# Performance work log

Hardware: AMD Instinct MI355X
Metric: run time of the kernel (lower is better)

The kernel has to match this reference:

```python
import jax, jax.numpy as jnp
import numpy as np

H, C = 8, 640            # n_heads, sentence_size (per-head out channels)
HC = H * C               # 5120 concatenated head width
NS, NW, NSEC = 8192, 65536, 1024   # sentences, words, sections
EW, ES, ESEC = 131072, 262144, 16384
WORD, SENT, SECT = 300, 640, 512
FFN_HID = 2048


def setup_inputs() -> dict:
    key = jax.random.key(0)
    ks = jax.random.split(key, 32)
    f = lambda k, sh: (jax.random.normal(k, sh, jnp.float32) * 0.02)
    ri = jax.random.randint
    inp = {}
    inp['Hs'] = jax.random.normal(ks[0], (NS, SENT), jnp.float32)
    inp['Hw'] = jax.random.normal(ks[1], (NW, WORD), jnp.float32)
    inp['HS'] = jax.random.normal(ks[2], (NSEC, SECT), jnp.float32)
    # edge_index convention: row 0 = source nodes, row 1 = target (sentence) nodes
    inp['w2s'] = jnp.stack([ri(ks[3], (EW,), 0, NW), ri(ks[4], (EW,), 0, NS)]).astype(jnp.int32)
    inp['s2s'] = jnp.stack([ri(ks[5], (ES,), 0, NS), ri(ks[6], (ES,), 0, NS)]).astype(jnp.int32)
    inp['S2s'] = jnp.stack([ri(ks[7], (ESEC,), 0, NSEC), ri(ks[8], (ESEC,), 0, NS)]).astype(jnp.int32)
    # gat_w: bipartite (word -> sentence)
    inp['Ww_src'] = f(ks[9], (WORD, HC)); inp['Ww_dst'] = f(ks[10], (SENT, HC))
    inp['aw_src'] = f(ks[11], (H, C)); inp['aw_dst'] = f(ks[12], (H, C)); inp['bw'] = f(ks[13], (HC,))
    # gat_s: sentence -> sentence (shared lin for src/dst)
    inp['Ws'] = f(ks[14], (SENT, HC))
    inp['as_src'] = f(ks[15], (H, C)); inp['as_dst'] = f(ks[16], (H, C)); inp['bs'] = f(ks[17], (HC,))
    # gat_S: bipartite (section -> sentence)
    inp['WS_src'] = f(ks[18], (SECT, HC)); inp['WS_dst'] = f(ks[19], (SENT, HC))
    inp['aS_src'] = f(ks[20], (H, C)); inp['aS_dst'] = f(ks[21], (H, C)); inp['bS'] = f(ks[22], (HC,))
    # fusion gates
    inp['F1_w'] = f(ks[23], (2 * HC, HC)); inp['F1_b'] = f(ks[24], (HC,))
    inp['F2_w'] = f(ks[25], (2 * HC, HC)); inp['F2_b'] = f(ks[26], (HC,))
    # FFN
    inp['l1_w'] = f(ks[27], (HC, FFN_HID)); inp['l1_b'] = f(ks[28], (FFN_HID,))
    inp['l2_w'] = f(ks[29], (FFN_HID, SENT)); inp['l2_b'] = f(ks[30], (SENT,))
    return inp


def _gat(xs, xd, Wsrc, Wdst, asrc, adst, b, edge_index):
    """PyG-style GATConv (concat heads), bipartite (xs -> xd)."""
    N = xd.shape[0]
    hs = (xs @ Wsrc).reshape(-1, H, C)          # [Nsrc,H,C]
    hd = (xd @ Wdst).reshape(-1, H, C)          # [Ndst,H,C]
    al_s = jnp.einsum('nhc,hc->nh', hs, asrc)   # [Nsrc,H]
    al_d = jnp.einsum('nhc,hc->nh', hd, adst)   # [Ndst,H]
    src, dst = edge_index[0], edge_index[1]
    e = jax.nn.leaky_relu(al_s[src] + al_d[dst], negative_slope=0.2)  # [E,H]
    m = jax.ops.segment_max(e, dst, num_segments=N)                   # segment-stable softmax
    ex = jnp.exp(e - m[dst])
    den = jax.ops.segment_sum(ex, dst, num_segments=N)
    alpha = ex / (den[dst] + 1e-16)
    out = jax.ops.segment_sum(hs[src] * alpha[:, :, None], dst, num_segments=N)
    return out.reshape(N, HC) + b


def _fusion(X, Y, W, b):
    Z = jax.nn.sigmoid(jnp.concatenate([X, Y], axis=-1) @ W + b)
    return Z * X + (1.0 - Z) * Y


def reference(Hs, Hw, HS, w2s, s2s, S2s,
              Ww_src, Ww_dst, aw_src, aw_dst, bw,
              Ws, as_src, as_dst, bs,
              WS_src, WS_dst, aS_src, aS_dst, bS,
              F1_w, F1_b, F2_w, F2_b,
              l1_w, l1_b, l2_w, l2_b):
    Uw = jax.nn.elu(_gat(Hw, Hs, Ww_src, Ww_dst, aw_src, aw_dst, bw, w2s))
    Us = jax.nn.elu(_gat(Hs, Hs, Ws, Ws, as_src, as_dst, bs, s2s))
    US = jax.nn.elu(_gat(HS, Hs, WS_src, WS_dst, aS_src, aS_dst, bS, S2s))
    U1 = _fusion(Uw, Us, F1_w, F1_b)
    U2 = _fusion(U1, US, F2_w, F2_b)
    return (U2 @ l1_w + l1_b) @ l2_w + l2_b + Hs
```

## Files before the change

kernel.cpp:

```cpp
#include <hip/hip_runtime.h>
#include <cstdint>
#include <cstddef>

typedef __attribute__((ext_vector_type(8))) __bf16 bf16x8;
typedef __attribute__((ext_vector_type(4))) float f32x4;

static constexpr int kNS   = 8192;
static constexpr int kNW   = 65536;
static constexpr int kNSEC = 1024;
static constexpr int kEW   = 131072;
static constexpr int kES   = 262144;
static constexpr int kESEC = 16384;

__device__ __forceinline__ float eluf(float x)  { return x > 0.f ? x : (__expf(x) - 1.f); }
__device__ __forceinline__ float sigmf(float x) { return 1.f / (1.f + __expf(-x)); }

__device__ __forceinline__ void gload16(const __bf16* g, __bf16* l) {
  __builtin_amdgcn_global_load_lds((const __attribute__((address_space(1))) unsigned int*)g,
                                   (__attribute__((address_space(3))) unsigned int*)l,
                                   16, 0, 0);
}

__global__ __launch_bounds__(256) void conv_transpose(const float* __restrict__ W, int K, int N,
                                                      __bf16* __restrict__ Wt, int KP) {
  __shared__ float t[64][33];
  const int nb = blockIdx.x * 32, kb = blockIdx.y * 64;
  const int tx = threadIdx.x & 31, ty = threadIdx.x >> 5;
#pragma unroll
  for (int i = ty; i < 64; i += 8) {
    const int k = kb + i;
    t[i][tx] = (k < K) ? W[(long)k * N + nb + tx] : 0.f;
  }
  __syncthreads();
  union BU { __bf16 b; unsigned short u; };
#pragma unroll
  for (int i = ty; i < 32; i += 8) {
    BU b0, b1;
    b0.b = (__bf16)t[tx * 2][i];
    b1.b = (__bf16)t[tx * 2 + 1][i];
    const unsigned int pk = ((unsigned int)b1.u << 16) | b0.u;
    *(unsigned int*)(Wt + (long)(nb + i) * KP + kb + tx * 2) = pk;
  }
}

__global__ __launch_bounds__(256) void conv_bf(const float* __restrict__ in, __bf16* __restrict__ outb, long n) {
  long i = (long)blockIdx.x * blockDim.x + threadIdx.x;
  if (i < n) outb[i] = (__bf16)in[i];
}

struct HVJ { const float* W; const float* a; float* o; int Kd; int KP; };
struct HVJobs { HVJ j[6]; };

__global__ __launch_bounds__(256) void head_vecs6(HVJobs jb) {
  const HVJ J = jb.j[blockIdx.z];
  const int h = blockIdx.x;
  const int lane = threadIdx.x & 63;
  const int k = blockIdx.y * 4 + (threadIdx.x >> 6);
  if (k >= J.KP) return;
  float s = 0.f;
  if (k < J.Kd) {
    const float* wr = J.W + (long)k * 5120 + h * 640;
    const float* ar = J.a + h * 640;
    for (int c = lane; c < 640; c += 64) s += wr[c] * ar[c];
  }
  for (int o2 = 32; o2; o2 >>= 1) s += __shfl_down(s, o2);
  if (lane == 0) J.o[h * J.KP + k] = (k < J.Kd) ? s : 0.f;
}

__global__ __launch_bounds__(256) void comb_bias(const float* __restrict__ l1_b, const float* __restrict__ l2_w,
                                                 const float* __restrict__ l2_b, float* __restrict__ bc) {
  const int n = blockIdx.x * 256 + threadIdx.x;
  if (n >= 640) return;
  float s = l2_b[n];
  for (int k = 0; k < 2048; ++k) s += l1_b[k] * l2_w[(long)k * 640 + n];
  bc[n] = s;
}

__global__ __launch_bounds__(256) void att_logits(const float* __restrict__ X, int ldx, int Kd,
                                                  const float* __restrict__ vec, int KP,
                                                  float* __restrict__ outl, int N) {
  const int lane = threadIdx.x & 63;
  const int node = blockIdx.x * 4 + (threadIdx.x >> 6);
  if (node >= N) return;
  const float* xr = X + (long)node * ldx;
  float p[8];
#pragma unroll
  for (int h = 0; h < 8; ++h) p[h] = 0.f;
  for (int k = lane; k < Kd; k += 64) {
    const float xv = xr[k];
#pragma unroll
    for (int h = 0; h < 8; ++h) p[h] += xv * vec[h * KP + k];
  }
#pragma unroll
  for (int h = 0; h < 8; ++h) {
    float v = p[h];
    for (int o2 = 32; o2; o2 >>= 1) v += __shfl_down(v, o2);
    if (lane == 0) outl[(long)node * 8 + h] = v;
  }
}

__global__ __launch_bounds__(256) void att_logits4(const float* __restrict__ X,
                                                   const float* __restrict__ v0, const float* __restrict__ v1,
                                                   const float* __restrict__ v2, const float* __restrict__ v3,
                                                   float* __restrict__ o0, float* __restrict__ o1,
                                                   float* __restrict__ o2, float* __restrict__ o3, int N) {
  const int lane = threadIdx.x & 63;
  const int node = blockIdx.x * 4 + (threadIdx.x >> 6);
  if (node >= N) return;
  const float* xr = X + (long)node * 640;
  float p[4][8];
#pragma unroll
  for (int s = 0; s < 4; ++s)
#pragma unroll
    for (int h = 0; h < 8; ++h) p[s][h] = 0.f;
  for (int k = lane; k < 640; k += 64) {
    const float xv = xr[k];
#pragma unroll
    for (int h = 0; h < 8; ++h) {
      p[0][h] += xv * v0[h * 640 + k];
      p[1][h] += xv * v1[h * 640 + k];
      p[2][h] += xv * v2[h * 640 + k];
      p[3][h] += xv * v3[h * 640 + k];
    }
  }
  float* outs[4] = {o0, o1, o2, o3};
#pragma unroll
  for (int s = 0; s < 4; ++s)
#pragma unroll
    for (int h = 0; h < 8; ++h) {
      float v = p[s][h];
      for (int o2v = 32; o2v; o2v >>= 1) v += __shfl_down(v, o2v);
      if (lane == 0) outs[s][(long)node * 8 + h] = v;
    }
}

__global__ __launch_bounds__(256) void edge_count3(const int* __restrict__ d0, int E0, int* __restrict__ c0,
                                                   const int* __restrict__ d1, int E1, int* __restrict__ c1,
                                                   const int* __restrict__ d2, int E2, int* __restrict__ c2) {
  const int gid = blockIdx.x * blockDim.x + threadIdx.x;
  if (gid < E0) atomicAdd(&c0[d0[gid]], 1);
  else if (gid < E0 + E1) atomicAdd(&c1[d1[gid - E0]], 1);
  else if (gid < E0 + E1 + E2) atomicAdd(&c2[d2[gid - E0 - E1]], 1);
}

__global__ __launch_bounds__(1024) void scan_off3(const int* __restrict__ c0, int* __restrict__ o0,
                                                  const int* __restrict__ c1, int* __restrict__ o1,
                                                  const int* __restrict__ c2, int* __restrict__ o2) {
  const int* cnt = blockIdx.x == 0 ? c0 : (blockIdx.x == 1 ? c1 : c2);
  int* offo = blockIdx.x == 0 ? o0 : (blockIdx.x == 1 ? o1 : o2);
  __shared__ int part[1024];
  const int tid = threadIdx.x;
  const int base = tid * 8;
  int loc[8];
  int s = 0;
#pragma unroll
  for (int i = 0; i < 8; ++i) { loc[i] = s; s += cnt[base + i]; }
  part[tid] = s;
  __syncthreads();
  for (int d2 = 1; d2 < 1024; d2 <<= 1) {
    int v = (tid >= d2) ? part[tid - d2] : 0;
    __syncthreads();
    part[tid] += v;
    __syncthreads();
  }
  const int pre = (tid > 0) ? part[tid - 1] : 0;
#pragma unroll
  for (int i = 0; i < 8; ++i) offo[base + i] = pre + loc[i];
  if (tid == 1023) offo[8192] = part[1023];
}

__global__ __launch_bounds__(256) void edge_fill3(
    const int* __restrict__ s0, const int* __restrict__ d0, int E0, const int* __restrict__ of0, int* __restrict__ cu0, int* __restrict__ sr0,
    const int* __restrict__ s1, const int* __restrict__ d1, int E1, const int* __restrict__ of1, int* __restrict__ cu1, int* __restrict__ sr1,
    const int* __restrict__ s2, const int* __restrict__ d2, int E2, const int* __restrict__ of2, int* __restrict__ cu2, int* __restrict__ sr2) {
  const int gid = blockIdx.x * blockDim.x + threadIdx.x;
  if (gid < E0) {
    const int d = d0[gid];
    sr0[of0[d] + atomicAdd(&cu0[d], 1)] = s0[gid];
  } else if (gid < E0 + E1) {
    const int g = gid - E0, d = d1[g];
    sr1[of1[d] + atomicAdd(&cu1[d], 1)] = s1[g];
  } else if (gid < E0 + E1 + E2) {
    const int g = gid - E0 - E1, d = d2[g];
    sr2[of2[d] + atomicAdd(&cu2[d], 1)] = s2[g];
  }
}

template <int FPAD, int F, bool XPH, bool BIASELU>
__global__ __launch_bounds__(256) void gat_agg(const int* __restrict__ seg_off, const int* __restrict__ ssrc,
                                               const float* __restrict__ als, const float* __restrict__ ald,
                                               const float* __restrict__ X, int ldx,
                                               __bf16* __restrict__ outp, int ldo,
                                               const float* __restrict__ bias) {
  constexpr int C4 = F / 4;
  constexpr int ITEMS = 8 * C4;
  constexpr int L = (ITEMS + 255) / 256;
  const int d = blockIdx.x;
  const int tid = threadIdx.x;
  const int o0 = seg_off[d], o1 = seg_off[d + 1];
  const int deg = o1 - o0;
  __shared__ float exl[64][8];
  __shared__ int ssl[64];
  __shared__ float aldd[8];
  __shared__ float den_s[8];
  if (tid < 8) { aldd[tid] = ald[(long)d * 8 + tid]; den_s[tid] = 0.f; }
  f32x4 acc[L];
  int hh[L], xo[L], oo[L];
  bool vld[L];
#pragma unroll
  for (int l = 0; l < L; ++l) {
    const int idx = tid + l * 256;
    vld[l] = (idx < ITEMS);
    const int h = vld[l] ? (idx / C4) : 0;
    const int c = vld[l] ? (idx - h * C4) : 0;
    hh[l] = h;
    xo[l] = (XPH ? h * F : 0) + c * 4;
    oo[l] = h * FPAD + c * 4;
#pragma unroll
    for (int r = 0; r < 4; ++r) acc[l][r] = 0.f;
  }
  __syncthreads();
  for (int base = 0; base < deg; base += 64) {
    const int nc = min(64, deg - base);
    if (tid < nc) ssl[tid] = ssrc[o0 + base + tid];
    __syncthreads();
    for (int t = tid; t < nc * 8; t += 256) {
      const int e = t >> 3, h = t & 7;
      float v = als[(long)ssl[e] * 8 + h] + aldd[h];
      v = v > 0.f ? v : 0.2f * v;
      exl[e][h] = __expf(v);
    }
    __syncthreads();
    if (tid < 8) {
      float s = 0.f;
      for (int e = 0; e < nc; ++e) s += exl[e][tid];
      den_s[tid] += s;
    }
    for (int e = 0; e < nc; ++e) {
      const float* xr = X + (long)ssl[e] * ldx;
      const float* ex8 = exl[e];
#pragma unroll
      for (int l = 0; l < L; ++l)
        if (vld[l]) {
          const f32x4 v = *(const f32x4*)(xr + xo[l]);
          acc[l] += ex8[hh[l]] * v;
        }
    }
    __syncthreads();
  }
#pragma unroll
  for (int l = 0; l < L; ++l) {
    if (!vld[l]) continue;
    const float dinv = 1.f / (den_s[hh[l]] + 1e-16f);
#pragma unroll
    for (int j = 0; j < 4; ++j) {
      float r = acc[l][j] * dinv;
      if constexpr (BIASELU) { r += bias[oo[l] + j]; r = eluf(r); }
      outp[(long)d * ldo + oo[l] + j] = (__bf16)r;
    }
  }
}

template <int FPAD, int F, bool XPH, bool BIASELU>
__global__ __launch_bounds__(256) void gat_agg_bf(const int* __restrict__ seg_off, const int* __restrict__ ssrc,
                                                  const float* __restrict__ als, const float* __restrict__ ald,
                                                  const __bf16* __restrict__ X, int ldx,
                                                  __bf16* __restrict__ outp, int ldo,
                                                  const float* __restrict__ bias) {
  constexpr int C8 = F / 8;
  constexpr int ITEMS = 8 * C8;
  constexpr int L = (ITEMS + 255) / 256;
  const int d = blockIdx.x;
  const int tid = threadIdx.x;
  const int o0 = seg_off[d], o1 = seg_off[d + 1];
  const int deg = o1 - o0;
  __shared__ float exl[64][8];
  __shared__ int ssl[64];
  __shared__ float aldd[8];
  __shared__ float den_s[8];
  if (tid < 8) { aldd[tid] = ald[(long)d * 8 + tid]; den_s[tid] = 0.f; }
  float acc[L][8];
  int hh[L], xo[L], oo[L];
  bool vld[L];
#pragma unroll
  for (int l = 0; l < L; ++l) {
    const int idx = tid + l * 256;
    vld[l] = (idx < ITEMS);
    const int h = vld[l] ? (idx / C8) : 0;
    const int c = vld[l] ? (idx - h * C8) : 0;
    hh[l] = h;
    xo[l] = (XPH ? h * F : 0) + c * 8;
    oo[l] = h * FPAD + c * 8;
#pragma unroll
    for (int r = 0; r < 8; ++r) acc[l][r] = 0.f;
  }
  __syncthreads();
  for (int base = 0; base < deg; base += 64) {
    const int nc = min(64, deg - base);
    if (tid < nc) ssl[tid] = ssrc[o0 + base + tid];
    __syncthreads();
    for (int t = tid; t < nc * 8; t += 256) {
      const int e = t >> 3, h = t & 7;
      float v = als[(long)ssl[e] * 8 + h] + aldd[h];
      v = v > 0.f ? v : 0.2f * v;
      exl[e][h] = __expf(v);
    }
    __syncthreads();
    if (tid < 8) {
      float s = 0.f;
      for (int e = 0; e < nc; ++e) s += exl[e][tid];
      den_s[tid] += s;
    }
    for (int e = 0; e < nc; ++e) {
      const __bf16* xr = X + (long)ssl[e] * ldx;
      const float* ex8 = exl[e];
#pragma unroll
      for (int l = 0; l < L; ++l)
        if (vld[l]) {
          const bf16x8 v = *(const bf16x8*)(xr + xo[l]);
          const float w = ex8[hh[l]];
#pragma unroll
          for (int r = 0; r < 8; ++r) acc[l][r] += w * (float)v[r];
        }
    }
    __syncthreads();
  }
#pragma unroll
  for (int l = 0; l < L; ++l) {
    if (!vld[l]) continue;
    const float dinv = 1.f / (den_s[hh[l]] + 1e-16f);
#pragma unroll
    for (int j = 0; j < 8; ++j) {
      float r = acc[l][j] * dinv;
      if constexpr (BIASELU) { r += bias[oo[l] + j]; r = eluf(r); }
      outp[(long)d * ldo + oo[l] + j] = (__bf16)r;
    }
  }
}

template <int EPI>
__global__ __launch_bounds__(256) void gemm_bt(
    const __bf16* __restrict__ A, int lda, const __bf16* __restrict__ A2, int ksplit,
    const __bf16* __restrict__ Bt, int ldb, int K,
    void* __restrict__ Cout, int ldc,
    const float* __restrict__ bias,
    const __bf16* __restrict__ Xg, const __bf16* __restrict__ Yg, int ldxy,
    const float* __restrict__ Res, int ldres,
    long a_zs, long bt_zs, long c_zs, int b_zs) {
  __shared__ __bf16 sA[2][128 * 32];
  __shared__ __bf16 sB[2][128 * 32];
  const int tid = threadIdx.x;
  const int z = blockIdx.z;
  const int m0 = blockIdx.y * 128, n0 = blockIdx.x * 128;
  const __bf16* Ab = A + (long)z * a_zs;
  const __bf16* A2b = A2 ? A2 + (long)z * a_zs : nullptr;
  const __bf16* Btb = Bt + (long)z * bt_zs;
  const int lane = tid & 63;
  const int wv = tid >> 6, wr = wv >> 1, wc = wv & 1;
  const int fr = lane & 15, fq = lane >> 4;

  const int r0 = tid >> 2, r1 = r0 + 64;
  const int csw = (((tid & 3) ^ ((r0 >> 1) & 3)) * 8);
  const int ldst0 = tid * 8;
  const int ldst1 = 2048 + tid * 8;

  f32x4 acc[4][4];
#pragma unroll
  for (int i = 0; i < 4; ++i)
#pragma unroll
    for (int j = 0; j < 4; ++j)
#pragma unroll
      for (int r = 0; r < 4; ++r) acc[i][j][r] = 0.f;

  const int fsw = (fq ^ ((fr >> 1) & 3)) * 8;
  int aof[4], bof[4];
#pragma unroll
  for (int i = 0; i < 4; ++i) {
    aof[i] = (wr * 64 + i * 16 + fr) * 32 + fsw;
    bof[i] = (wc * 64 + i * 16 + fr) * 32 + fsw;
  }

  const int nkt = K >> 5;
  auto stage = [&](int buf, int kt) {
    const int k0 = kt * 32;
    const __bf16* As = Ab;
    int kr = k0;
    if (A2b && k0 >= ksplit) { As = A2b; kr = k0 - ksplit; }
    gload16(As + (long)(m0 + r0) * lda + kr + csw, &sA[buf][ldst0]);
    gload16(As + (long)(m0 + r1) * lda + kr + csw, &sA[buf][ldst1]);
    gload16(Btb + (long)(n0 + r0) * ldb + k0 + csw, &sB[buf][ldst0]);
    gload16(Btb + (long)(n0 + r1) * ldb + k0 + csw, &sB[buf][ldst1]);
  };

  stage(0, 0);
  for (int kt = 0; kt < nkt; ++kt) {
    const int cur = kt & 1;
    __syncthreads();
    if (kt + 1 < nkt) stage(cur ^ 1, kt + 1);
    bf16x8 af[4], bfv[4];
#pragma unroll
    for (int i = 0; i < 4; ++i) {
      af[i] = *(const bf16x8*)(&sA[cur][aof[i]]);
      bfv[i] = *(const bf16x8*)(&sB[cur][bof[i]]);
    }
#pragma unroll
    for (int i = 0; i < 4; ++i)
#pragma unroll
      for (int j = 0; j < 4; ++j)
        acc[i][j] = __builtin_amdgcn_mfma_f32_16x16x32_bf16(af[i], bfv[j], acc[i][j], 0, 0, 0);
  }

  const float* biasb = bias ? bias + (long)z * b_zs : nullptr;
#pragma unroll
  for (int i = 0; i < 4; ++i) {
#pragma unroll
    for (int j = 0; j < 4; ++j) {
#pragma unroll
      for (int r = 0; r < 4; ++r) {
        const int mm = m0 + wr * 64 + i * 16 + fq * 4 + r;
        const int nn = n0 + wc * 64 + j * 16 + fr;
        const float v = acc[i][j][r];
        const long cidx = (long)mm * ldc + nn + (long)z * c_zs;
        if constexpr (EPI == 0) {
          ((float*)Cout)[cidx] = v;
        } else if constexpr (EPI == 1) {
          ((__bf16*)Cout)[cidx] = (__bf16)eluf(v + biasb[nn]);
        } else if constexpr (EPI == 2) {
          const float zt = sigmf(v + biasb[nn]);
          const float x = (float)Xg[(long)mm * ldxy + nn];
          const float y = (float)Yg[(long)mm * ldxy + nn];
          ((__bf16*)Cout)[cidx] = (__bf16)(zt * x + (1.f - zt) * y);
        } else if constexpr (EPI == 3) {
          ((__bf16*)Cout)[cidx] = (__bf16)(v + biasb[nn]);
        } else if constexpr (EPI == 4) {
          ((float*)Cout)[cidx] = v + biasb[nn] + Res[(long)mm * ldres + nn];
        } else {
          ((__bf16*)Cout)[cidx] = (__bf16)v;
        }
      }
    }
  }
}

template <int EPI>
__global__ __launch_bounds__(512, 2) void gemm256(
    const __bf16* __restrict__ A, int lda, const __bf16* __restrict__ A2, int ksplit,
    const __bf16* __restrict__ Bt, int ldb, int K,
    void* __restrict__ Cout, int ldc,
    const float* __restrict__ bias,
    const __bf16* __restrict__ Xg, const __bf16* __restrict__ Yg, int ldxy,
    int nn_tiles) {
  __shared__ __bf16 sA[2][2][256 * 32];
  __shared__ __bf16 sB[2][2][256 * 32];
  const int tid = threadIdx.x;

  const int nwg = gridDim.x;
  const int lin = blockIdx.x;
  const int qq = nwg >> 3, rr = nwg & 7;
  const int xcd = lin & 7, pos = lin >> 3;
  const int swz = (xcd < rr ? xcd * (qq + 1) : rr * (qq + 1) + (xcd - rr) * qq) + pos;
  const int m0 = (swz / nn_tiles) * 256;
  const int n0 = (swz % nn_tiles) * 256;

  const int lane = tid & 63;
  const int wv = tid >> 6, wm = wv >> 2, wn = wv & 3;
  const int fr = lane & 15, fq = lane >> 4;

  const int srow = tid >> 2;
  const int pslot = tid & 3;

  auto stageA = [&](int bp, int tt, int kk) {
    const int kcol0 = tt * 64 + kk * 32;
    const __bf16* src = A;
    int kc = kcol0;
    if (A2 && kcol0 >= ksplit) { src = A2; kc = kcol0 - ksplit; }
    __bf16* dst = &sA[bp][kk][0];
#pragma unroll
    for (int i = 0; i < 2; ++i) {
      const int r = i * 128 + srow;
      const int l = pslot ^ ((r >> 1) & 3);
      gload16(src + (long)(m0 + r) * lda + kc + l * 8, dst + (i * 512 + tid) * 8);
    }
  };
  auto stageB = [&](int bp, int tt, int kk) {
    const int kcol0 = tt * 64 + kk * 32;
    __bf16* dst = &sB[bp][kk][0];
#pragma unroll
    for (int i = 0; i < 2; ++i) {
      const int r = i * 128 + srow;
      const int l = pslot ^ ((r >> 1) & 3);
      gload16(Bt + (long)(n0 + r) * ldb + kcol0 + l * 8, dst + (i * 512 + tid) * 8);
    }
  };

  int aoff[8], boff[4];
#pragma unroll
  for (int mf = 0; mf < 8; ++mf) {
    const int ra = wm * 128 + mf * 16 + fr;
    aoff[mf] = ra * 32 + ((fq ^ ((ra >> 1) & 3)) * 8);
  }
#pragma unroll
  for (int nf = 0; nf < 4; ++nf) {
    const int rb = wn * 64 + nf * 16 + fr;
    boff[nf] = rb * 32 + ((fq ^ ((rb >> 1) & 3)) * 8);
  }

  f32x4 acc[8][4];
#pragma unroll
  for (int i = 0; i < 8; ++i)
#pragma unroll
    for (int j = 0; j < 4; ++j)
#pragma unroll
      for (int r = 0; r < 4; ++r) acc[i][j][r] = 0.f;

  const int nkt = K >> 6;

  bf16x8 aA[4], aB[4], bA[4], bB[4];

  stageA(0, 0, 0); stageB(0, 0, 0); stageA(0, 0, 1); stageB(0, 0, 1);
  asm volatile("s_waitcnt vmcnt(4)" ::: "memory");
  __builtin_amdgcn_s_barrier();
#pragma unroll
  for (int mf = 0; mf < 4; ++mf) aA[mf] = *(const bf16x8*)(&sA[0][0][aoff[mf]]);
#pragma unroll
  for (int nf = 0; nf < 4; ++nf) bA[nf] = *(const bf16x8*)(&sB[0][0][boff[nf]]);

  for (int t = 0; t < nkt; ++t) {
    const int cb = t & 1, nb = cb ^ 1;
    const bool pf = (t + 1 < nkt);

#pragma unroll
    for (int mf = 0; mf < 4; ++mf) aB[mf] = *(const bf16x8*)(&sA[cb][0][aoff[4 + mf]]);
    if (pf) stageA(nb, t + 1, 0);
    asm volatile("s_waitcnt lgkmcnt(4)" ::: "memory");
    __builtin_amdgcn_sched_barrier(0);
    __builtin_amdgcn_s_setprio(1);
#pragma unroll
    for (int mf = 0; mf < 4; ++mf)
#pragma unroll
      for (int nf = 0; nf < 4; ++nf)
        acc[mf][nf] = __builtin_amdgcn_mfma_f32_16x16x32_bf16(aA[mf], bA[nf], acc[mf][nf], 0, 0, 0);
    __builtin_amdgcn_s_setprio(0);
    __builtin_amdgcn_sched_barrier(0);

    if (pf) stageB(nb, t + 1, 0);
    if (pf) asm volatile("s_waitcnt vmcnt(4)" ::: "memory");
    else    asm volatile("s_waitcnt vmcnt(0)" ::: "memory");
    __builtin_amdgcn_s_barrier();

#pragma unroll
    for (int mf = 0; mf < 4; ++mf) aA[mf] = *(const bf16x8*)(&sA[cb][1][aoff[mf]]);
#pragma unroll
    for (int nf = 0; nf < 4; ++nf) bB[nf] = *(const bf16x8*)(&sB[cb][1][boff[nf]]);
    asm volatile("s_waitcnt lgkmcnt(8)" ::: "memory");
    __builtin_amdgcn_sched_barrier(0);
    __builtin_amdgcn_s_setprio(1);
#pragma unroll
    for (int mf = 0; mf < 4; ++mf)
#pragma unroll
      for (int nf = 0; nf < 4; ++nf)
        acc[4 + mf][nf] = __builtin_amdgcn_mfma_f32_16x16x32_bf16(aB[mf], bA[nf], acc[4 + mf][nf], 0, 0, 0);
    __builtin_amdgcn_s_setprio(0);
    __builtin_amdgcn_sched_barrier(0);

#pragma unroll
    for (int mf = 0; mf < 4; ++mf) aB[mf] = *(const bf16x8*)(&sA[cb][1][aoff[4 + mf]]);
    if (pf) stageA(nb, t + 1, 1);
    asm volatile("s_waitcnt lgkmcnt(4)" ::: "memory");
    __builtin_amdgcn_sched_barrier(0);
    __builtin_amdgcn_s_setprio(1);
#pragma unroll
    for (int mf = 0; mf < 4; ++mf)
#pragma unroll
      for (int nf = 0; nf < 4; ++nf)
        acc[mf][nf] = __builtin_amdgcn_mfma_f32_16x16x32_bf16(aA[mf], bB[nf], acc[mf][nf], 0, 0, 0);
    __builtin_amdgcn_s_setprio(0);
    __builtin_amdgcn_sched_barrier(0);

    if (pf) {
      stageB(nb, t + 1, 1);
      asm volatile("s_waitcnt vmcnt(4)" ::: "memory");
    }
    __builtin_amdgcn_s_barrier();

    if (pf) {
#pragma unroll
      for (int mf = 0; mf < 4; ++mf) aA[mf] = *(const bf16x8*)(&sA[nb][0][aoff[mf]]);
#pragma unroll
      for (int nf = 0; nf < 4; ++nf) bA[nf] = *(const bf16x8*)(&sB[nb][0][boff[nf]]);
      asm volatile("s_waitcnt lgkmcnt(8)" ::: "memory");
    } else {
      asm volatile("s_waitcnt lgkmcnt(0)" ::: "memory");
    }
    __builtin_amdgcn_sched_barrier(0);
    __builtin_amdgcn_s_setprio(1);
#pragma unroll
    for (int mf = 0; mf < 4; ++mf)
#pragma unroll
      for (int nf = 0; nf < 4; ++nf)
        acc[4 + mf][nf] = __builtin_amdgcn_mfma_f32_16x16x32_bf16(aB[mf], bB[nf], acc[4 + mf][nf], 0, 0, 0);
    __builtin_amdgcn_s_setprio(0);
    __builtin_amdgcn_sched_barrier(0);
  }

#pragma unroll
  for (int mf = 0; mf < 8; ++mf) {
#pragma unroll
    for (int nf = 0; nf < 4; ++nf) {
#pragma unroll
      for (int r = 0; r < 4; ++r) {
        const int mm = m0 + wm * 128 + mf * 16 + fq * 4 + r;
        const int nn = n0 + wn * 64 + nf * 16 + fr;
        const float v = acc[mf][nf][r];
        const long cidx = (long)mm * ldc + nn;
        if constexpr (EPI == 2) {
          const float zt = sigmf(v + bias[nn]);
          const float x = (float)Xg[(long)mm * ldxy + nn];
          const float y = (float)Yg[(long)mm * ldxy + nn];
          ((__bf16*)Cout)[cidx] = (__bf16)(zt * x + (1.f - zt) * y);
        } else {
          ((__bf16*)Cout)[cidx] = (__bf16)(v + bias[nn]);
        }
      }
    }
  }
}

extern "C" void kernel_launch(void* const* d_in, const int* in_sizes, int n_in,
                              void* d_out, int out_size, void* d_ws, size_t ws_size,
                              hipStream_t stream) {
  (void)in_sizes; (void)n_in; (void)out_size; (void)ws_size;
  const float* Hs    = (const float*)d_in[0];
  const float* Hw    = (const float*)d_in[1];
  const float* HSec  = (const float*)d_in[2];
  const int* w2s     = (const int*)d_in[3];
  const int* s2s     = (const int*)d_in[4];
  const int* S2s     = (const int*)d_in[5];
  const float* Ww_src = (const float*)d_in[6];
  const float* Ww_dst = (const float*)d_in[7];
  const float* aw_src = (const float*)d_in[8];
  const float* aw_dst = (const float*)d_in[9];
  const float* bw     = (const float*)d_in[10];
  const float* Wss    = (const float*)d_in[11];
  const float* as_src = (const float*)d_in[12];
  const float* as_dst = (const float*)d_in[13];
  const float* bs     = (const float*)d_in[14];
  const float* WS_src = (const float*)d_in[15];
  const float* WS_dst = (const float*)d_in[16];
  const float* aS_src = (const float*)d_in[17];
  const float* aS_dst = (const float*)d_in[18];
  const float* bS     = (const float*)d_in[19];
  const float* F1_w   = (const float*)d_in[20];
  const float* F1_b   = (const float*)d_in[21];
  const float* F2_w   = (const float*)d_in[22];
  const float* F2_b   = (const float*)d_in[23];
  const float* l1_w   = (const float*)d_in[24];
  const float* l1_b   = (const float*)d_in[25];
  const float* l2_w   = (const float*)d_in[26];
  const float* l2_b   = (const float*)d_in[27];
  float* outp = (float*)d_out;

  char* ws = (char*)d_ws;
  size_t cur_off = 0;
  auto alloc = [&](size_t bytes) -> char* {
    char* p = ws + cur_off;
    cur_off = (cur_off + bytes + 255) & ~(size_t)255;
    return p;
  };

  __bf16* Wt_w  = (__bf16*)alloc((size_t)5120 * 320 * 2);
  __bf16* Wt_s  = (__bf16*)alloc((size_t)5120 * 640 * 2);
  __bf16* Wt_S  = (__bf16*)alloc((size_t)5120 * 512 * 2);
  __bf16* WtF   = (__bf16*)alloc((size_t)5120 * 10240 * 2);
  __bf16* Wt_l2 = (__bf16*)alloc((size_t)640 * 2048 * 2);
  __bf16* l1_bf = (__bf16*)alloc((size_t)5120 * 2048 * 2);
  __bf16* WcT   = (__bf16*)alloc((size_t)640 * 5120 * 2);
  float*  bc    = (float*)alloc(640 * 4);
  __bf16* HS_bf = (__bf16*)alloc((size_t)1024 * 512 * 2);
  __bf16* Hs_bf = (__bf16*)alloc((size_t)kNS * 640 * 2);
  float* v_w = (float*)alloc(8 * 320 * 4);
  float* u_w = (float*)alloc(8 * 640 * 4);
  float* v_s = (float*)alloc(8 * 640 * 4);
  float* u_s = (float*)alloc(8 * 640 * 4);
  float* v_S = (float*)alloc(8 * 512 * 4);
  float* u_S = (float*)alloc(8 * 640 * 4);
  float* alw_s = (float*)alloc((size_t)kNW * 8 * 4);
  float* alw_d = (float*)alloc((size_t)kNS * 8 * 4);
  float* als_s = (float*)alloc((size_t)kNS * 8 * 4);
  float* als_d = (float*)alloc((size_t)kNS * 8 * 4);
  float* alS_s = (float*)alloc((size_t)kNSEC * 8 * 4);
  float* alS_d = (float*)alloc((size_t)kNS * 8 * 4);
  int* csr_i  = (int*)alloc((size_t)6 * kNS * 4);
  int* cnt_w = csr_i, *cnt_s = csr_i + kNS, *cnt_S = csr_i + 2 * kNS;
  int* cur_w = csr_i + 3 * kNS, *cur_s = csr_i + 4 * kNS, *cur_S = csr_i + 5 * kNS;
  int* off_w = (int*)alloc((size_t)(kNS + 1) * 4);
  int* off_s = (int*)alloc((size_t)(kNS + 1) * 4);
  int* off_S = (int*)alloc((size_t)(kNS + 1) * 4);
  int* ssrc_w = (int*)alloc((size_t)kEW * 4);
  int* ssrc_s = (int*)alloc((size_t)kES * 4);
  int* ssrc_S = (int*)alloc((size_t)kESEC * 4);
  __bf16* hs_Sb = (__bf16*)alloc((size_t)1024 * 5120 * 2);
  char* aggreg = alloc((size_t)kNS * 2560 * 2 + (size_t)kNS * 5120 * 2);
  __bf16* agg_w = (__bf16*)aggreg;
  __bf16* agg_s = (__bf16*)(aggreg + (size_t)kNS * 2560 * 2);
  __bf16* U1 = (__bf16*)aggreg;
  __bf16* Uw = (__bf16*)alloc((size_t)kNS * 5120 * 2);
  __bf16* Us = (__bf16*)alloc((size_t)kNS * 5120 * 2);
  __bf16* US = (__bf16*)alloc((size_t)kNS * 5120 * 2);
  __bf16* U2 = Uw;

  const dim3 b256(256);

  conv_transpose<<<dim3(160, 5), b256, 0, stream>>>(Ww_src, 300, 5120, Wt_w, 320);
  conv_transpose<<<dim3(160, 10), b256, 0, stream>>>(Wss, 640, 5120, Wt_s, 640);
  conv_transpose<<<dim3(160, 8), b256, 0, stream>>>(WS_src, 512, 5120, Wt_S, 512);
  conv_transpose<<<dim3(160, 160), b256, 0, stream>>>(F1_w, 10240, 5120, WtF, 10240);
  conv_transpose<<<dim3(20, 32), b256, 0, stream>>>(l2_w, 2048, 640, Wt_l2, 2048);
  conv_bf<<<(1024 * 512 + 255) / 256, b256, 0, stream>>>(HSec, HS_bf, (long)1024 * 512);
  conv_bf<<<((long)kNS * 640 + 255) / 256, b256, 0, stream>>>(Hs, Hs_bf, (long)kNS * 640);
  conv_bf<<<((long)5120 * 2048 + 255) / 256, b256, 0, stream>>>(l1_w, l1_bf, (long)5120 * 2048);

  gemm_bt<5><<<dim3(40, 5, 1), b256, 0, stream>>>(
      Wt_l2, 2048, nullptr, 1 << 30, l1_bf, 2048, 2048,
      WcT, 5120, nullptr, nullptr, nullptr, 0, nullptr, 0, 0, 0, 0, 0);
  comb_bias<<<3, b256, 0, stream>>>(l1_b, l2_w, l2_b, bc);

  {
    HVJobs jb;
    jb.j[0] = {Ww_src, aw_src, v_w, 300, 320};
    jb.j[1] = {Ww_dst, aw_dst, u_w, 640, 640};
    jb.j[2] = {Wss,    as_src, v_s, 640, 640};
    jb.j[3] = {Wss,    as_dst, u_s, 640, 640};
    jb.j[4] = {WS_src, aS_src, v_S, 512, 512};
    jb.j[5] = {WS_dst, aS_dst, u_S, 640, 640};
    head_vecs6<<<dim3(8, 160, 6), b256, 0, stream>>>(jb);
  }

  att_logits<<<(kNW + 3) / 4, b256, 0, stream>>>(Hw, 300, 300, v_w, 320, alw_s, kNW);
  att_logits<<<(kNSEC + 3) / 4, b256, 0, stream>>>(HSec, 512, 512, v_S, 512, alS_s, kNSEC);
  att_logits4<<<(kNS + 3) / 4, b256, 0, stream>>>(Hs, u_w, v_s, u_s, u_S,
                                                  alw_d, als_s, als_d, alS_d, kNS);

  hipMemsetAsync(csr_i, 0, (size_t)6 * kNS * 4, stream);
  edge_count3<<<(kEW + kES + kESEC + 255) / 256, b256, 0, stream>>>(
      w2s + kEW, kEW, cnt_w, s2s + kES, kES, cnt_s, S2s + kESEC, kESEC, cnt_S);
  scan_off3<<<3, 1024, 0, stream>>>(cnt_w, off_w, cnt_s, off_s, cnt_S, off_S);
  edge_fill3<<<(kEW + kES + kESEC + 255) / 256, b256, 0, stream>>>(
      w2s, w2s + kEW, kEW, off_w, cur_w, ssrc_w,
      s2s, s2s + kES, kES, off_s, cur_s, ssrc_s,
      S2s, S2s + kESEC, kESEC, off_S, cur_S, ssrc_S);

  gemm_bt<5><<<dim3(40, 8, 1), b256, 0, stream>>>(
      HS_bf, 512, nullptr, 1 << 30, Wt_S, 512, 512,
      hs_Sb, 5120, nullptr, nullptr, nullptr, 0, nullptr, 0, 0, 0, 0, 0);

  gat_agg<320, 300, false, false><<<kNS, b256, 0, stream>>>(off_w, ssrc_w, alw_s, alw_d, Hw, 300, agg_w, 2560, nullptr);
  gat_agg_bf<640, 640, false, false><<<kNS, b256, 0, stream>>>(off_s, ssrc_s, als_s, als_d, Hs_bf, 640, agg_s, 5120, nullptr);
  gat_agg_bf<640, 640, true, true><<<kNS, b256, 0, stream>>>(off_S, ssrc_S, alS_s, alS_d, hs_Sb, 5120, US, 5120, bS);

  gemm_bt<1><<<dim3(5, 64, 8), b256, 0, stream>>>(
      agg_w, 2560, nullptr, 1 << 30, Wt_w, 320, 320,
      Uw, 5120, bw, nullptr, nullptr, 0, nullptr, 0, 320, (long)640 * 320, 640, 640);
  gemm_bt<1><<<dim3(5, 64, 8), b256, 0, stream>>>(
      agg_s, 5120, nullptr, 1 << 30, Wt_s, 640, 640,
      Us, 5120, bs, nullptr, nullptr, 0, nullptr, 0, 640, (long)640 * 640, 640, 640);

  gemm256<2><<<dim3(640), dim3(512), 0, stream>>>(
      Uw, 5120, Us, 5120, WtF, 10240, 10240,
      U1, 5120, F1_b, Uw, Us, 5120, 20);

  conv_transpose<<<dim3(160, 160), b256, 0, stream>>>(F2_w, 10240, 5120, WtF, 10240);
  gemm256<2><<<dim3(640), dim3(512), 0, stream>>>(
      U1, 5120, US, 5120, WtF, 10240, 10240,
      U2, 5120, F2_b, U1, US, 5120, 20);

  gemm_bt<4><<<dim3(5, 64, 1), b256, 0, stream>>>(
      U2, 5120, nullptr, 1 << 30, WcT, 5120, 5120,
      outp, 640, bc, nullptr, nullptr, 0, Hs, 640, 0, 0, 0, 0);
}
```

Before: 2.982 ms.

## Vectorize fp32-to-bf16 conversion, parallelize combined bias, pre-transpose F2 weights

The elementwise bf16 conversion now handles four floats per thread using 16-byte loads and 8-byte stores. The combined-bias reduction is split across 20 blocks, with 8 k-slices per block reduced through shared memory, where it previously ran on 3 blocks. When the workspace has room, F2_w is transposed into its own buffer up front so it no longer sits serially between the two fusion GEMMs. The cost is extra workspace, and the transpose still runs inside the same stream.

```diff
diff --git a/kernel.cpp b/kernel.cpp
--- a/kernel.cpp
+++ b/kernel.cpp
@@ -43,9 +43,14 @@
   }
 }
 
-__global__ __launch_bounds__(256) void conv_bf(const float* __restrict__ in, __bf16* __restrict__ outb, long n) {
-  long i = (long)blockIdx.x * blockDim.x + threadIdx.x;
-  if (i < n) outb[i] = (__bf16)in[i];
+__global__ __launch_bounds__(256) void conv_bf4(const float* __restrict__ in, __bf16* __restrict__ outb, long n4) {
+  const long i = (long)blockIdx.x * blockDim.x + threadIdx.x;
+  if (i >= n4) return;
+  const f32x4 v = *(const f32x4*)(in + i * 4);
+  union { __bf16 b[4]; uint2 u; } p;
+  p.b[0] = (__bf16)v[0]; p.b[1] = (__bf16)v[1];
+  p.b[2] = (__bf16)v[2]; p.b[3] = (__bf16)v[3];
+  *(uint2*)(outb + i * 4) = p.u;
 }
 
 struct HVJ { const float* W; const float* a; float* o; int Kd; int KP; };
@@ -69,11 +74,21 @@
 
 __global__ __launch_bounds__(256) void comb_bias(const float* __restrict__ l1_b, const float* __restrict__ l2_w,
                                                  const float* __restrict__ l2_b, float* __restrict__ bc) {
-  const int n = blockIdx.x * 256 + threadIdx.x;
-  if (n >= 640) return;
-  float s = l2_b[n];
-  for (int k = 0; k < 2048; ++k) s += l1_b[k] * l2_w[(long)k * 640 + n];
-  bc[n] = s;
+  __shared__ float red[8][32];
+  const int no = threadIdx.x & 31;
+  const int ko = threadIdx.x >> 5;
+  const int n = blockIdx.x * 32 + no;
+  float s = 0.f;
+  for (int k = ko; k < 2048; k += 8) s += l1_b[k] * l2_w[(long)k * 640 + n];
+  red[ko][no] = s;
+  __syncthreads();
+  if (threadIdx.x < 32) {
+    const int nn = blockIdx.x * 32 + threadIdx.x;
+    float t = l2_b[nn];
+#pragma unroll
+    for (int i = 0; i < 8; ++i) t += red[i][threadIdx.x];
+    bc[nn] = t;
+  }
 }
 
 __global__ __launch_bounds__(256) void att_logits(const float* __restrict__ X, int ldx, int Kd,
@@ -629,7 +644,7 @@
 extern "C" void kernel_launch(void* const* d_in, const int* in_sizes, int n_in,
                               void* d_out, int out_size, void* d_ws, size_t ws_size,
                               hipStream_t stream) {
-  (void)in_sizes; (void)n_in; (void)out_size; (void)ws_size;
+  (void)in_sizes; (void)n_in; (void)out_size;
   const float* Hs    = (const float*)d_in[0];
   const float* Hw    = (const float*)d_in[1];
   const float* HSec  = (const float*)d_in[2];
@@ -709,21 +724,28 @@
   __bf16* US = (__bf16*)alloc((size_t)kNS * 5120 * 2);
   __bf16* U2 = Uw;
 
+  __bf16* WtF2 = nullptr;
+  {
+    const size_t f2b = (size_t)5120 * 10240 * 2;
+    if (cur_off + f2b + 256 <= ws_size) WtF2 = (__bf16*)alloc(f2b);
+  }
+
   const dim3 b256(256);
 
   conv_transpose<<<dim3(160, 5), b256, 0, stream>>>(Ww_src, 300, 5120, Wt_w, 320);
   conv_transpose<<<dim3(160, 10), b256, 0, stream>>>(Wss, 640, 5120, Wt_s, 640);
   conv_transpose<<<dim3(160, 8), b256, 0, stream>>>(WS_src, 512, 5120, Wt_S, 512);
   conv_transpose<<<dim3(160, 160), b256, 0, stream>>>(F1_w, 10240, 5120, WtF, 10240);
+  if (WtF2) conv_transpose<<<dim3(160, 160), b256, 0, stream>>>(F2_w, 10240, 5120, WtF2, 10240);
   conv_transpose<<<dim3(20, 32), b256, 0, stream>>>(l2_w, 2048, 640, Wt_l2, 2048);
-  conv_bf<<<(1024 * 512 + 255) / 256, b256, 0, stream>>>(HSec, HS_bf, (long)1024 * 512);
-  conv_bf<<<((long)kNS * 640 + 255) / 256, b256, 0, stream>>>(Hs, Hs_bf, (long)kNS * 640);
-  conv_bf<<<((long)5120 * 2048 + 255) / 256, b256, 0, stream>>>(l1_w, l1_bf, (long)5120 * 2048);
+  conv_bf4<<<(1024 * 512 / 4 + 255) / 256, b256, 0, stream>>>(HSec, HS_bf, (long)1024 * 512 / 4);
+  conv_bf4<<<((long)kNS * 640 / 4 + 255) / 256, b256, 0, stream>>>(Hs, Hs_bf, (long)kNS * 640 / 4);
+  conv_bf4<<<((long)5120 * 2048 / 4 + 255) / 256, b256, 0, stream>>>(l1_w, l1_bf, (long)5120 * 2048 / 4);
 
   gemm_bt<5><<<dim3(40, 5, 1), b256, 0, stream>>>(
       Wt_l2, 2048, nullptr, 1 << 30, l1_bf, 2048, 2048,
       WcT, 5120, nullptr, nullptr, nullptr, 0, nullptr, 0, 0, 0, 0, 0);
-  comb_bias<<<3, b256, 0, stream>>>(l1_b, l2_w, l2_b, bc);
+  comb_bias<<<20, b256, 0, stream>>>(l1_b, l2_w, l2_b, bc);
 
   {
     HVJobs jb;
@@ -769,9 +791,9 @@
       Uw, 5120, Us, 5120, WtF, 10240, 10240,
       U1, 5120, F1_b, Uw, Us, 5120, 20);
 
-  conv_transpose<<<dim3(160, 160), b256, 0, stream>>>(F2_w, 10240, 5120, WtF, 10240);
+  if (!WtF2) conv_transpose<<<dim3(160, 160), b256, 0, stream>>>(F2_w, 10240, 5120, WtF, 10240);
   gemm256<2><<<dim3(640), dim3(512), 0, stream>>>(
-      U1, 5120, US, 5120, WtF, 10240, 10240,
+      U1, 5120, US, 5120, WtF2 ? WtF2 : WtF, 10240, 10240,
       U2, 5120, F2_b, U1, US, 5120, 20);
 
   gemm_bt<4><<<dim3(5, 64, 1), b256, 0, stream>>>(
```

New measurement: 2.875 ms, median of 2. -3.6%, faster.
